# Kernel tuning notes

Hardware: AMD Instinct MI355X
Metric: run time of the kernel (lower is better)

## Reference

```python
import jax, jax.numpy as jnp
import numpy as np

B, D, H, O, RH, P = 8192, 784, 2048, 1024, 128, 64
NI = NJ = NK = 4  # input regions / hidden groups / output groups


def _make_groups():
    idx = np.arange(28 * 28).reshape(28, 28)
    input_groups = np.stack([
        idx[:14, :14].ravel(), idx[:14, 14:].ravel(),
        idx[14:, :14].ravel(), idx[14:, 14:].ravel(),
    ]).astype(np.int32)                                   # [4, 196]
    hidden_groups = np.arange(H, dtype=np.int32).reshape(NJ, H // NJ)   # [4, 512]
    output_groups = np.arange(O, dtype=np.int32).reshape(NK, O // NK)   # [4, 256]
    return input_groups, hidden_groups, output_groups


def setup_inputs() -> dict:
    key = jax.random.key(0)
    ks = jax.random.split(key, 9)
    ig, hg, og = _make_groups()
    inp = {
        "x":   jax.random.normal(ks[0], (B, D), jnp.float32),
        "W1":  jax.random.normal(ks[1], (H, D), jnp.float32) / np.sqrt(D),
        "b1":  jax.random.normal(ks[2], (H,), jnp.float32) * 0.01,
        "W2":  jax.random.normal(ks[3], (O, H), jnp.float32) / np.sqrt(H),
        "b2":  jax.random.normal(ks[4], (O,), jnp.float32) * 0.01,
        "Wr1": jax.random.normal(ks[5], (RH, D), jnp.float32) / np.sqrt(D),
        "br1": jax.random.normal(ks[6], (RH,), jnp.float32) * 0.01,
        "Wr2": jax.random.normal(ks[7], (P, RH), jnp.float32) / np.sqrt(RH),
        "br2": jax.random.normal(ks[8], (P,), jnp.float32) * 0.01,
        "input_groups": jnp.asarray(ig),
        "hidden_groups": jnp.asarray(hg),
        "output_groups": jnp.asarray(og),
        "top_k": 8,
    }
    return inp


def reference(x, W1, b1, W2, b2, Wr1, br1, Wr2, br2,
              input_groups, hidden_groups, output_groups, top_k):
    # --- router MLP (eval mode: dropout = identity, no routing noise) ---
    h_r = jax.nn.relu(x @ Wr1.T + br1)
    scores = h_r @ Wr2.T + br2                      # [B, P]
    probs = jax.nn.softmax(scores, axis=-1)         # temperature = 1.0

    # --- top-k pathway selection + renormalization ---
    top_vals, top_idx = jax.lax.top_k(probs, top_k)
    bsz = x.shape[0]
    mask = jnp.zeros_like(probs).at[jnp.arange(bsz)[:, None], top_idx].set(top_vals)
    wts = mask / (mask.sum(axis=-1, keepdims=True) + 1e-8)
    wts4 = wts.reshape(bsz, NI, NJ, NK)             # pathway_idx = i*16 + j*4 + k

    # --- gather pathway sub-blocks ---
    x_reg = x[:, input_groups]                      # [B, I, 196]
    # W1g[i, j] = W1[hidden_groups[j]][:, input_groups[i]] -> [I, J, 512, 196]
    W1g = W1[hidden_groups[None, :, :, None], input_groups[:, None, None, :]]
    b1g = b1[hidden_groups]                         # [J, 512]
    # W2g[j, k] = W2[output_groups[k]][:, hidden_groups[j]] -> [J, K, 256, 512]
    W2g = W2[output_groups[None, :, :, None], hidden_groups[:, None, None, :]]
    b2g = b2[output_groups]                         # [K, 256]

    # --- pathway computation (exact erf GELU, as torch F.gelu default) ---
    hidden = jax.nn.gelu(
        jnp.einsum('bin,ijhn->ijbh', x_reg, W1g) + b1g[None, :, None, :],
        approximate=False)                          # [I, J, B, 512]
    # weighted pathway outputs, contracted over i, j, h without materializing
    # the full [I, J, K, B, 256] tensor
    out_main = jnp.einsum('ijbh,jkoh,bijk->bko', hidden, W2g, wts4)  # [B, K, 256]
    wsum = wts4.sum(axis=(1, 2))                    # [B, K] (bias weighted per pathway)
    out_blocks = out_main + wsum[:, :, None] * b2g[None]

    out = jnp.zeros((bsz, O), x.dtype).at[:, output_groups].add(out_blocks)
    return out
```

## Files before the change

### kernel.cpp

```cpp
#include <hip/hip_runtime.h>
#include <hip/hip_bf16.h>
#include <hip/hip_fp16.h>

#define B_  8192
#define D_  784
#define H_  2048
#define O_  1024
#define RH_ 128
#define P_  64
#define KP  224
#define KC  196

typedef __attribute__((ext_vector_type(8))) short short8;
typedef __attribute__((ext_vector_type(4))) float f32x4;

__device__ inline float bf2f(unsigned short u) {
  union { unsigned int i; float f; } v; v.i = ((unsigned int)u) << 16; return v.f;
}
__device__ inline unsigned short f2bf(float f) {
  __hip_bfloat16 h = __float2bfloat16(f);
  return *reinterpret_cast<unsigned short*>(&h);
}
__device__ inline unsigned short f2h(float f) {
  __half h = __float2half(f);
  return *reinterpret_cast<unsigned short*>(&h);
}
__device__ inline float h2f(unsigned short u) {
  __half h = *reinterpret_cast<__half*>(&u);
  return __half2float(h);
}
__device__ inline float erf_fast(float x) {
  float ax = fabsf(x);
  float t = 1.0f / (1.0f + 0.3275911f * ax);
  float p = ((((1.061405429f * t - 1.453152027f) * t + 1.421413741f) * t
              - 0.284496736f) * t + 0.254829592f) * t;
  float y = 1.0f - p * __expf(-ax * ax);
  return x < 0.f ? -y : y;
}
__device__ inline float gelu_exact(float v) {
  return 0.5f * v * (1.0f + erf_fast(v * 0.70710678118654752f));
}

__device__ inline void gload_lds16(const void* g, void* l) {
  __builtin_amdgcn_global_load_lds((const __attribute__((address_space(1))) void*)g,
                                   (__attribute__((address_space(3))) void*)l, 16, 0, 0);
}

__device__ inline void gemm128_db(const unsigned short* gA0, const unsigned short* gA1,
                                  const unsigned short* gB0, const unsigned short* gB1,
                                  int K, char* lds, f32x4 acc[4][4]) {
  const int t = threadIdx.x;
  const int w = t >> 6, l = t & 63;
  const int wr = (w >> 1) * 64, wc = (w & 1) * 64;
  const int lr = l & 15;
  const int swr = (lr >> 1) & 3;
  const int arow = (wr + lr) * 64 + (((l >> 4) ^ swr) * 16);
  const int brow = 8192 + (wc + lr) * 64 + (((l >> 4) ^ swr) * 16);
  const int tOff = t * 16;
  {
    char* d = lds + tOff;
    gload_lds16(gA0, d);
    gload_lds16(gA1, d + 4096);
    gload_lds16(gB0, d + 8192);
    gload_lds16(gB1, d + 12288);
  }
  __syncthreads();
  int cur = 0;
  for (int kt = 0; kt < K; kt += 32) {
    const int nxt = kt + 32;
    if (nxt < K) {
      char* d = lds + ((cur ^ 1) << 14) + tOff;
      gload_lds16(gA0 + nxt, d);
      gload_lds16(gA1 + nxt, d + 4096);
      gload_lds16(gB0 + nxt, d + 8192);
      gload_lds16(gB1 + nxt, d + 12288);
    }
    __builtin_amdgcn_sched_barrier(0);
    const char* buf = lds + (cur << 14);
    short8 af[4], bfr[4];
#pragma unroll
    for (int f = 0; f < 4; ++f) {
      af[f]  = *(const short8*)(buf + arow + f * 1024);
      bfr[f] = *(const short8*)(buf + brow + f * 1024);
    }
#pragma unroll
    for (int fm = 0; fm < 4; ++fm)
#pragma unroll
      for (int fn = 0; fn < 4; ++fn)
        acc[fm][fn] = __builtin_amdgcn_mfma_f32_16x16x32_bf16(af[fm], bfr[fn], acc[fm][fn], 0, 0, 0);
    __syncthreads();
    cur ^= 1;
  }
}

__device__ inline void gemm128_db64(const unsigned short* gA0, const unsigned short* gA1,
                                    const unsigned short* gB0, const unsigned short* gB1,
                                    int K, char* lds, f32x4 acc[4][4]) {
  const int t = threadIdx.x;
  const int w = t >> 6, l = t & 63;
  const int wr = (w >> 1) * 64, wc = (w & 1) * 64;
  const int lr = l & 15;
  const int swr = (lr >> 1) & 3;
  const int arow = (wr + lr) * 64 + (((l >> 4) ^ swr) * 16);
  const int brow = 8192 + (wc + lr) * 64 + (((l >> 4) ^ swr) * 16);
  const int tOff = t * 16;
#define STAGE64(bufbase, ksrc) { \
    char* d = lds + (bufbase) + tOff; \
    gload_lds16(gA0 + (ksrc), d); \
    gload_lds16(gA1 + (ksrc), d + 4096); \
    gload_lds16(gB0 + (ksrc), d + 8192); \
    gload_lds16(gB1 + (ksrc), d + 12288); \
    gload_lds16(gA0 + (ksrc) + 32, d + 16384); \
    gload_lds16(gA1 + (ksrc) + 32, d + 16384 + 4096); \
    gload_lds16(gB0 + (ksrc) + 32, d + 16384 + 8192); \
    gload_lds16(gB1 + (ksrc) + 32, d + 16384 + 12288); \
  }
  STAGE64(0, 0);
  __syncthreads();
  int cur = 0;
  for (int kt = 0; kt < K; kt += 64) {
    if (kt + 64 < K) STAGE64((cur ^ 1) << 15, kt + 64);
    __builtin_amdgcn_sched_barrier(0);
    const char* buf = lds + (cur << 15);
#pragma unroll
    for (int c = 0; c < 2; ++c) {
      const char* ch = buf + c * 16384;
      short8 af[4], bfr[4];
#pragma unroll
      for (int f = 0; f < 4; ++f) {
        af[f]  = *(const short8*)(ch + arow + f * 1024);
        bfr[f] = *(const short8*)(ch + brow + f * 1024);
      }
#pragma unroll
      for (int fm = 0; fm < 4; ++fm)
#pragma unroll
        for (int fn = 0; fn < 4; ++fn)
          acc[fm][fn] = __builtin_amdgcn_mfma_f32_16x16x32_bf16(af[fm], bfr[fn], acc[fm][fn], 0, 0, 0);
    }
    __syncthreads();
    cur ^= 1;
  }
#undef STAGE64
}

__device__ inline void gemm128_bt64(const unsigned short* __restrict__ A,
                                    const unsigned short* __restrict__ Bm,
                                    int K, char* lds, f32x4 acc[4][4]) {
  const int t = threadIdx.x;
  const int s_orig = (t & 3) ^ ((t >> 3) & 3);
  const size_t srcOff = (size_t)(t >> 2) * K + s_orig * 8;
  gemm128_db64(A + srcOff, A + srcOff + (size_t)64 * K,
               Bm + srcOff, Bm + srcOff + (size_t)64 * K, K, lds, acc);
}

__global__ void k_prep(const float* __restrict__ x, const float* __restrict__ W1,
                       const float* __restrict__ W2, const int* __restrict__ ig,
                       unsigned short* __restrict__ xreg, unsigned short* __restrict__ w1g,
                       unsigned short* __restrict__ w2b) {
  const size_t N1 = (size_t)4 * B_ * KP;
  const size_t N2 = (size_t)4 * H_ * KP;
  const size_t N3 = (size_t)O_ * H_;
  const size_t TOT = N1 + N2 + N3;
  for (size_t idx = (size_t)blockIdx.x * blockDim.x + threadIdx.x; idx < TOT;
       idx += (size_t)gridDim.x * blockDim.x) {
    if (idx < N1) {
      int n = (int)(idx % KP); size_t r = idx / KP;
      int b = (int)(r % B_); int i = (int)(r / B_);
      float v = (n < 196) ? x[(size_t)b * D_ + ig[i * 196 + n]] : 0.f;
      xreg[idx] = f2bf(v);
    } else if (idx < N1 + N2) {
      size_t q = idx - N1;
      int n = (int)(q % KP); size_t r = q / KP;
      int h = (int)(r % H_); int i = (int)(r / H_);
      float v = (n < 196) ? W1[(size_t)h * D_ + ig[i * 196 + n]] : 0.f;
      w1g[q] = f2bf(v);
    } else {
      size_t q = idx - N1 - N2;
      w2b[q] = f2bf(W2[q]);
    }
  }
}

__global__ __launch_bounds__(256) void k_r1s(const float* __restrict__ x,
    const float* __restrict__ Wr1, const float* __restrict__ br1,
    float* __restrict__ hrp) {
  __shared__ float As[64][33];
  __shared__ float Bs[64][33];
  const int b0 = blockIdx.x * 64;
  const int h0 = blockIdx.y * 64;
  const int kb = blockIdx.z * KC;
  const int kend = kb + KC;
  const int t = threadIdx.x;
  const int srow = t >> 2;
  const int scol = (t & 3) * 8;
  const int ty = t >> 4, tx = t & 15;
  float acc[4][4];
#pragma unroll
  for (int i = 0; i < 4; ++i)
#pragma unroll
    for (int j = 0; j < 4; ++j) acc[i][j] = 0.f;
  const float* gA = x   + (size_t)(b0 + srow) * D_;
  const float* gB = Wr1 + (size_t)(h0 + srow) * D_;
  float4 a0 = *(const float4*)(gA + kb + scol);
  float4 a1 = *(const float4*)(gA + kb + scol + 4);
  float4 w0 = *(const float4*)(gB + kb + scol);
  float4 w1 = *(const float4*)(gB + kb + scol + 4);
  for (int k0 = kb; k0 < kend; k0 += 32) {
    __syncthreads();
    *(float4*)&As[srow][scol]     = a0;
    *(float4*)&As[srow][scol + 4] = a1;
    *(float4*)&Bs[srow][scol]     = w0;
    *(float4*)&Bs[srow][scol + 4] = w1;
    __syncthreads();
    const int kn = k0 + 32;
    if (kn < kend) {
      a0 = (kn + scol + 4 <= kend) ? *(const float4*)(gA + kn + scol)     : float4{0,0,0,0};
      a1 = (kn + scol + 8 <= kend) ? *(const float4*)(gA + kn + scol + 4) : float4{0,0,0,0};
      w0 = (kn + scol + 4 <= kend) ? *(const float4*)(gB + kn + scol)     : float4{0,0,0,0};
      w1 = (kn + scol + 8 <= kend) ? *(const float4*)(gB + kn + scol + 4) : float4{0,0,0,0};
    }
    __builtin_amdgcn_sched_barrier(0);
#pragma unroll
    for (int kk = 0; kk < 8; ++kk) {
      float4 a4[4], b4[4];
#pragma unroll
      for (int i = 0; i < 4; ++i) a4[i] = *(const float4*)&As[ty * 4 + i][kk * 4];
#pragma unroll
      for (int j = 0; j < 4; ++j) b4[j] = *(const float4*)&Bs[tx * 4 + j][kk * 4];
#pragma unroll
      for (int i = 0; i < 4; ++i)
#pragma unroll
        for (int j = 0; j < 4; ++j)
          acc[i][j] += a4[i].x * b4[j].x + a4[i].y * b4[j].y +
                       a4[i].z * b4[j].z + a4[i].w * b4[j].w;
    }
  }
  float* hz = hrp + (size_t)blockIdx.z * B_ * RH_;
#pragma unroll
  for (int j = 0; j < 4; ++j) {
    const int h = h0 + tx * 4 + j;
    const float bias = (blockIdx.z == 0) ? br1[h] : 0.f;
#pragma unroll
    for (int i = 0; i < 4; ++i)
      hz[(size_t)(b0 + ty * 4 + i) * RH_ + h] = acc[i][j] + bias;
  }
}

#define R2S 32
__global__ __launch_bounds__(256) void k_r2(const float* __restrict__ hrp,
    const float* __restrict__ Wr2, const float* __restrict__ br2,
    float* __restrict__ wts, float* __restrict__ wsum,
    unsigned long long* __restrict__ actmask) {
  __shared__ float Ws[64][130];
  __shared__ float hs[R2S][128];
  const int s0 = blockIdx.x * R2S;
  const int t = threadIdx.x;
  for (int idx = t; idx < 2048; idx += 256) {
    int r = idx >> 5, c = (idx & 31) * 4;
    *(float4*)&Ws[r][c] = *(const float4*)(Wr2 + (size_t)r * RH_ + c);
  }
  for (int idx = t; idx < R2S * 32; idx += 256) {
    int r = idx >> 5, c = (idx & 31) * 4;
    const size_t off = (size_t)(s0 + r) * RH_ + c;
    float4 p0 = *(const float4*)(hrp + off);
    float4 p1 = *(const float4*)(hrp + (size_t)1 * B_ * RH_ + off);
    float4 p2 = *(const float4*)(hrp + (size_t)2 * B_ * RH_ + off);
    float4 p3 = *(const float4*)(hrp + (size_t)3 * B_ * RH_ + off);
    float4 s;
    s.x = fmaxf(p0.x + p1.x + p2.x + p3.x, 0.f);
    s.y = fmaxf(p0.y + p1.y + p2.y + p3.y, 0.f);
    s.z = fmaxf(p0.z + p1.z + p2.z + p3.z, 0.f);
    s.w = fmaxf(p0.w + p1.w + p2.w + p3.w, 0.f);
    *(float4*)&hs[r][c] = s;
  }
  __syncthreads();
  const int w = t >> 6, p = t & 63;
  const float wb2 = br2[p];
  for (int si = 0; si < R2S / 4; ++si) {
    const int sl = w * (R2S / 4) + si;
    float sc = wb2;
#pragma unroll
    for (int kk = 0; kk < 32; ++kk) {
      float4 h4 = *(const float4*)&hs[sl][kk * 4];
      float4 w4 = *(const float4*)&Ws[p][kk * 4];
      sc += h4.x * w4.x + h4.y * w4.y + h4.z * w4.z + h4.w * w4.w;
    }
    float m = sc;
#pragma unroll
    for (int o = 32; o; o >>= 1) m = fmaxf(m, __shfl_xor(m, o));
    float e = __expf(sc - m);
    float Z = e;
#pragma unroll
    for (int o = 32; o; o >>= 1) Z += __shfl_xor(Z, o);
    bool sel = false;
    float ssum = 0.f;
    for (int it = 0; it < 8; ++it) {
      float v = sel ? -1.f : e;
      float vm = v;
#pragma unroll
      for (int o = 32; o; o >>= 1) vm = fmaxf(vm, __shfl_xor(vm, o));
      unsigned long long mask = __ballot(!sel && v == vm);
      int first = __ffsll((long long)mask) - 1;
      if (p == first) sel = true;
      ssum += vm;
    }
    const float dn = 1.0f / (ssum + 1e-8f * Z);
    const float wv = sel ? e * dn : 0.f;
    wts[(size_t)(s0 + sl) * 64 + p] = wv;
    const unsigned long long am = __ballot(sel);
    if (p == 0) actmask[s0 + sl] = am;
    float part = wv;
#pragma unroll
    for (int o = 4; o < 64; o <<= 1) part += __shfl_xor(part, o);
    if (p < 4) wsum[(size_t)(s0 + sl) * 4 + p] = part;
  }
}

__global__ __launch_bounds__(256) void k_compact(const unsigned long long* __restrict__ actmask,
                                                 int* __restrict__ lists,
                                                 int* __restrict__ counts) {
  __shared__ int wcnt[4];
  __shared__ int sbase;
  const int ij = blockIdx.x;
  const int shift = (ij >> 2) * 16 + (ij & 3) * 4;
  const int t = threadIdx.x;
  const int wid = t >> 6, lane = t & 63;
  unsigned long long mk[32];
#pragma unroll
  for (int c = 0; c < 32; ++c) mk[c] = actmask[c * 256 + t];
  if (t == 0) sbase = 0;
  __syncthreads();
  for (int c = 0; c < 32; ++c) {
    const int b = c * 256 + t;
    const bool act = ((mk[c] >> shift) & 0xFULL) != 0ULL;
    const unsigned long long m = __ballot(act);
    if (lane == 0) wcnt[wid] = __popcll(m);
    __syncthreads();
    int off = sbase;
    const int tot = wcnt[0] + wcnt[1] + wcnt[2] + wcnt[3];
    for (int q = 0; q < wid; ++q) off += wcnt[q];
    if (act)
      lists[ij * B_ + off + __popcll(m & ((1ULL << lane) - 1ULL))] = b;
    __syncthreads();
    if (t == 0) sbase += tot;
  }
  __syncthreads();
  if (t == 0) counts[ij] = sbase;
}

__global__ __launch_bounds__(256) void k_l1g(const unsigned short* __restrict__ xreg,
    const unsigned short* __restrict__ w1g, const float* __restrict__ b1,
    const int* __restrict__ lists, const int* __restrict__ counts,
    unsigned short* __restrict__ hid16) {
  const int mt = blockIdx.x, nt = blockIdx.y, iq = blockIdx.z;
  const int ij = iq * 4 + (nt >> 2);
  const int count = counts[ij];
  if (mt * 128 >= count) return;
  __shared__ __align__(128) char lds[32768];
  __shared__ int rows[128];
  const int t = threadIdx.x;
  const int* list = lists + (size_t)ij * B_;
  if (t < 128) {
    int rl = mt * 128 + t;
    rows[t] = list[rl < count ? rl : count - 1];
  }
  __syncthreads();
  const int s_orig = (t & 3) ^ ((t >> 3) & 3);
  const int scol = s_orig * 8;
  const int r0 = rows[t >> 2], r1 = rows[(t >> 2) + 64];
  const unsigned short* gA0 = xreg + ((size_t)iq * B_ + r0) * KP + scol;
  const unsigned short* gA1 = xreg + ((size_t)iq * B_ + r1) * KP + scol;
  const unsigned short* gB0 = w1g + ((size_t)(iq * H_ + nt * 128) + (t >> 2)) * KP + scol;
  const unsigned short* gB1 = gB0 + (size_t)64 * KP;
  f32x4 acc[4][4];
#pragma unroll
  for (int a = 0; a < 4; ++a)
#pragma unroll
    for (int b = 0; b < 4; ++b) acc[a][b] = (f32x4){0.f, 0.f, 0.f, 0.f};
  gemm128_db(gA0, gA1, gB0, gB1, KP, lds, acc);
  const int w = t >> 6, l = t & 63;
  const int rloc0 = (w >> 1) * 64 + (l >> 4) * 4;
  const int cloc = (w & 1) * 64 + (l & 15);
  unsigned short* lt = (unsigned short*)lds;
#pragma unroll
  for (int fn = 0; fn < 4; ++fn) {
    const int col = cloc + fn * 16;
    const float bias = b1[nt * 128 + col];
#pragma unroll
    for (int fm = 0; fm < 4; ++fm)
#pragma unroll
      for (int r = 0; r < 4; ++r) {
        const int row = rloc0 + fm * 16 + r;
        const int gsw = (col >> 3) ^ (row & 7);
        lt[row * 128 + gsw * 8 + (col & 7)] = f2h(acc[fm][fn][r] + bias);
      }
  }
  __syncthreads();
  const int mlim = count - mt * 128;
  const int row = t >> 1, half = t & 1;
  if (row < mlim) {
    unsigned short* dst = hid16 + ((size_t)iq * B_ + rows[row]) * H_ + nt * 128 + half * 64;
#pragma unroll
    for (int q = 0; q < 8; ++q) {
      const int g = (half * 8 + q) ^ (row & 7);
      *(short8*)(dst + q * 8) = *(const short8*)(lt + row * 128 + g * 8);
    }
  }
}

__global__ __launch_bounds__(256) void k_combine(unsigned short* __restrict__ hid,
                                                 const float* __restrict__ wts) {
  const int b = blockIdx.x;
  const int n = threadIdx.x * 8;
  const int j = n >> 9;
  const float* wb = wts + (size_t)b * 64 + j * 4;
  float acc[4][8];
#pragma unroll
  for (int k = 0; k < 4; ++k)
#pragma unroll
    for (int e = 0; e < 8; ++e) acc[k][e] = 0.f;
#pragma unroll
  for (int i = 0; i < 4; ++i) {
    const float4 w4 = *(const float4*)(wb + i * 16);
    if (w4.x != 0.f || w4.y != 0.f || w4.z != 0.f || w4.w != 0.f) {
      short8 raw = *(const short8*)(hid + ((size_t)i * B_ + b) * H_ + n);
#pragma unroll
      for (int e = 0; e < 8; ++e) {
        float g = gelu_exact(h2f((unsigned short)raw[e]));
        acc[0][e] += g * w4.x;
        acc[1][e] += g * w4.y;
        acc[2][e] += g * w4.z;
        acc[3][e] += g * w4.w;
      }
    }
  }
#pragma unroll
  for (int k = 0; k < 4; ++k) {
    short8 outv;
#pragma unroll
    for (int e = 0; e < 8; ++e) outv[e] = (short)f2bf(acc[k][e]);
    *(short8*)(hid + ((size_t)k * B_ + b) * H_ + n) = outv;
  }
}

__global__ __launch_bounds__(256) void k_l2(const unsigned short* __restrict__ G,
    const unsigned short* __restrict__ w2b, const float* __restrict__ b2,
    const float* __restrict__ wsum, float* __restrict__ out) {
  __shared__ __align__(128) char lds[65536];
  const int mt = blockIdx.x, nt = blockIdx.y, k = blockIdx.z;
  const unsigned short* A  = G + ((size_t)k * B_ + mt * 128) * H_;
  const unsigned short* Bm = w2b + ((size_t)(k * 256 + nt * 128)) * H_;
  f32x4 acc[4][4];
#pragma unroll
  for (int a = 0; a < 4; ++a)
#pragma unroll
    for (int b = 0; b < 4; ++b) acc[a][b] = (f32x4){0.f, 0.f, 0.f, 0.f};
  gemm128_bt64(A, Bm, H_, lds, acc);
  const int t = threadIdx.x, w = t >> 6, l = t & 63;
  const int rbase = mt * 128 + (w >> 1) * 64 + (l >> 4) * 4;
  const int cb = nt * 128 + (w & 1) * 64 + (l & 15);
#pragma unroll
  for (int fn = 0; fn < 4; ++fn) {
    const int ncol = k * 256 + cb + fn * 16;
    const float bias = b2[ncol];
#pragma unroll
    for (int fm = 0; fm < 4; ++fm)
#pragma unroll
      for (int r = 0; r < 4; ++r) {
        const int m = rbase + fm * 16 + r;
        out[(size_t)m * O_ + ncol] = acc[fm][fn][r] + wsum[m * 4 + k] * bias;
      }
  }
}

extern "C" void kernel_launch(void* const* d_in, const int* in_sizes, int n_in,
                              void* d_out, int out_size, void* d_ws, size_t ws_size,
                              hipStream_t stream) {
  const float* x   = (const float*)d_in[0];
  const float* W1  = (const float*)d_in[1];
  const float* b1  = (const float*)d_in[2];
  const float* W2  = (const float*)d_in[3];
  const float* b2  = (const float*)d_in[4];
  const float* Wr1 = (const float*)d_in[5];
  const float* br1 = (const float*)d_in[6];
  const float* Wr2 = (const float*)d_in[7];
  const float* br2 = (const float*)d_in[8];
  const int*   ig  = (const int*)d_in[9];
  float* out = (float*)d_out;
  char* ws = (char*)d_ws;
  unsigned short* xreg = (unsigned short*)(ws);
  unsigned short* w1g  = (unsigned short*)(ws + 14680064);
  unsigned short* w2b  = (unsigned short*)(ws + 18350080);
  float*          wts  = (float*)(ws + 22544384);
  float*          wsum = (float*)(ws + 24641536);
  unsigned short* hid  = (unsigned short*)(ws + 24772608);
  float*          hrp  = (float*)(ws + 24772608);
  int*                lists   = (int*)d_out;
  int*                counts  = lists + 16 * B_;
  unsigned long long* actmask = (unsigned long long*)((char*)d_out + 524352);

  k_prep<<<dim3(2048), dim3(256), 0, stream>>>(x, W1, W2, ig, xreg, w1g, w2b);
  k_r1s<<<dim3(B_ / 64, RH_ / 64, 4), dim3(256), 0, stream>>>(x, Wr1, br1, hrp);
  k_r2<<<dim3(B_ / R2S), dim3(256), 0, stream>>>(hrp, Wr2, br2, wts, wsum, actmask);
  k_compact<<<dim3(16), dim3(256), 0, stream>>>(actmask, lists, counts);
  k_l1g<<<dim3(B_ / 128, H_ / 128, 4), dim3(256), 0, stream>>>(xreg, w1g, b1, lists, counts, hid);
  k_combine<<<dim3(B_), dim3(256), 0, stream>>>(hid, wts);
  k_l2<<<dim3(B_ / 128, 2, 4), dim3(256), 0, stream>>>(hid, w2b, b2, wsum, out);
}
```

Before: 234.8 us.

## Compute router first layer with split-fp16 MFMA instead of fp32 FMA

Replaces the scalar fp32 router GEMM with an MFMA-based one. x and Wr1 are each split into hi and lo fp16 parts, and three products (xhi*Whi, xlo*Whi, xhi*Wlo) are computed as separate z-slices, which keeps near-fp32 accuracy. The router bias is now added in k_r2 instead of the GEMM, and the prep kernel writes the padded split operands. This costs extra prep work and workspace memory, in exchange for matrix-core throughput on the router matmul.

Measured after the change: 209.4 us. -10.8%, faster.

```diff
diff --git a/kernel.cpp b/kernel.cpp
--- a/kernel.cpp
+++ b/kernel.cpp
@@ -9,9 +9,10 @@
 #define RH_ 128
 #define P_  64
 #define KP  224
-#define KC  196
+#define KR  800
 
 typedef __attribute__((ext_vector_type(8))) short short8;
+typedef __attribute__((ext_vector_type(8))) _Float16 h16x8;
 typedef __attribute__((ext_vector_type(4))) float f32x4;
 
 __device__ inline float bf2f(unsigned short u) {
@@ -46,6 +47,7 @@
                                    (__attribute__((address_space(3))) void*)l, 16, 0, 0);
 }
 
+template <bool F16>
 __device__ inline void gemm128_db(const unsigned short* gA0, const unsigned short* gA1,
                                   const unsigned short* gB0, const unsigned short* gB1,
                                   int K, char* lds, f32x4 acc[4][4]) {
@@ -86,8 +88,13 @@
 #pragma unroll
     for (int fm = 0; fm < 4; ++fm)
 #pragma unroll
-      for (int fn = 0; fn < 4; ++fn)
-        acc[fm][fn] = __builtin_amdgcn_mfma_f32_16x16x32_bf16(af[fm], bfr[fn], acc[fm][fn], 0, 0, 0);
+      for (int fn = 0; fn < 4; ++fn) {
+        if constexpr (F16)
+          acc[fm][fn] = __builtin_amdgcn_mfma_f32_16x16x32_f16(
+              (h16x8)af[fm], (h16x8)bfr[fn], acc[fm][fn], 0, 0, 0);
+        else
+          acc[fm][fn] = __builtin_amdgcn_mfma_f32_16x16x32_bf16(af[fm], bfr[fn], acc[fm][fn], 0, 0, 0);
+      }
     __syncthreads();
     cur ^= 1;
   }
@@ -155,12 +162,16 @@
 
 __global__ void k_prep(const float* __restrict__ x, const float* __restrict__ W1,
                        const float* __restrict__ W2, const int* __restrict__ ig,
+                       const float* __restrict__ Wr1,
                        unsigned short* __restrict__ xreg, unsigned short* __restrict__ w1g,
-                       unsigned short* __restrict__ w2b) {
+                       unsigned short* __restrict__ w2b,
+                       unsigned short* __restrict__ xsp, unsigned short* __restrict__ wr1sp) {
   const size_t N1 = (size_t)4 * B_ * KP;
   const size_t N2 = (size_t)4 * H_ * KP;
   const size_t N3 = (size_t)O_ * H_;
-  const size_t TOT = N1 + N2 + N3;
+  const size_t N4 = (size_t)B_ * KR;
+  const size_t N5 = (size_t)RH_ * KR;
+  const size_t TOT = N1 + N2 + N3 + N4 + N5;
   for (size_t idx = (size_t)blockIdx.x * blockDim.x + threadIdx.x; idx < TOT;
        idx += (size_t)gridDim.x * blockDim.x) {
     if (idx < N1) {
@@ -174,80 +185,66 @@
       int h = (int)(r % H_); int i = (int)(r / H_);
       float v = (n < 196) ? W1[(size_t)h * D_ + ig[i * 196 + n]] : 0.f;
       w1g[q] = f2bf(v);
-    } else {
+    } else if (idx < N1 + N2 + N3) {
       size_t q = idx - N1 - N2;
       w2b[q] = f2bf(W2[q]);
-    }
-  }
-}
-
-__global__ __launch_bounds__(256) void k_r1s(const float* __restrict__ x,
-    const float* __restrict__ Wr1, const float* __restrict__ br1,
-    float* __restrict__ hrp) {
-  __shared__ float As[64][33];
-  __shared__ float Bs[64][33];
-  const int b0 = blockIdx.x * 64;
-  const int h0 = blockIdx.y * 64;
-  const int kb = blockIdx.z * KC;
-  const int kend = kb + KC;
-  const int t = threadIdx.x;
-  const int srow = t >> 2;
-  const int scol = (t & 3) * 8;
-  const int ty = t >> 4, tx = t & 15;
-  float acc[4][4];
-#pragma unroll
-  for (int i = 0; i < 4; ++i)
-#pragma unroll
-    for (int j = 0; j < 4; ++j) acc[i][j] = 0.f;
-  const float* gA = x   + (size_t)(b0 + srow) * D_;
-  const float* gB = Wr1 + (size_t)(h0 + srow) * D_;
-  float4 a0 = *(const float4*)(gA + kb + scol);
-  float4 a1 = *(const float4*)(gA + kb + scol + 4);
-  float4 w0 = *(const float4*)(gB + kb + scol);
-  float4 w1 = *(const float4*)(gB + kb + scol + 4);
-  for (int k0 = kb; k0 < kend; k0 += 32) {
-    __syncthreads();
-    *(float4*)&As[srow][scol]     = a0;
-    *(float4*)&As[srow][scol + 4] = a1;
-    *(float4*)&Bs[srow][scol]     = w0;
-    *(float4*)&Bs[srow][scol + 4] = w1;
-    __syncthreads();
-    const int kn = k0 + 32;
-    if (kn < kend) {
-      a0 = (kn + scol + 4 <= kend) ? *(const float4*)(gA + kn + scol)     : float4{0,0,0,0};
-      a1 = (kn + scol + 8 <= kend) ? *(const float4*)(gA + kn + scol + 4) : float4{0,0,0,0};
-      w0 = (kn + scol + 4 <= kend) ? *(const float4*)(gB + kn + scol)     : float4{0,0,0,0};
-      w1 = (kn + scol + 8 <= kend) ? *(const float4*)(gB + kn + scol + 4) : float4{0,0,0,0};
-    }
-    __builtin_amdgcn_sched_barrier(0);
-#pragma unroll
-    for (int kk = 0; kk < 8; ++kk) {
-      float4 a4[4], b4[4];
-#pragma unroll
-      for (int i = 0; i < 4; ++i) a4[i] = *(const float4*)&As[ty * 4 + i][kk * 4];
-#pragma unroll
-      for (int j = 0; j < 4; ++j) b4[j] = *(const float4*)&Bs[tx * 4 + j][kk * 4];
-#pragma unroll
-      for (int i = 0; i < 4; ++i)
-#pragma unroll
-        for (int j = 0; j < 4; ++j)
-          acc[i][j] += a4[i].x * b4[j].x + a4[i].y * b4[j].y +
-                       a4[i].z * b4[j].z + a4[i].w * b4[j].w;
-    }
-  }
-  float* hz = hrp + (size_t)blockIdx.z * B_ * RH_;
-#pragma unroll
-  for (int j = 0; j < 4; ++j) {
-    const int h = h0 + tx * 4 + j;
-    const float bias = (blockIdx.z == 0) ? br1[h] : 0.f;
-#pragma unroll
-    for (int i = 0; i < 4; ++i)
-      hz[(size_t)(b0 + ty * 4 + i) * RH_ + h] = acc[i][j] + bias;
+    } else if (idx < N1 + N2 + N3 + N4) {
+      size_t q = idx - N1 - N2 - N3;
+      int c = (int)(q % KR); int b = (int)(q / KR);
+      float v = (c < D_) ? x[(size_t)b * D_ + c] : 0.f;
+      unsigned short hi = f2h(v);
+      unsigned short lo = f2h(v - h2f(hi));
+      xsp[(size_t)b * (2 * KR) + c]      = hi;
+      xsp[(size_t)b * (2 * KR) + KR + c] = lo;
+    } else {
+      size_t q = idx - N1 - N2 - N3 - N4;
+      int c = (int)(q % KR); int h = (int)(q / KR);
+      float v = (c < D_) ? Wr1[(size_t)h * D_ + c] : 0.f;
+      unsigned short hi = f2h(v);
+      unsigned short lo = f2h(v - h2f(hi));
+      wr1sp[(size_t)h * KR + c]                    = hi;
+      wr1sp[(size_t)RH_ * KR + h * KR + c]         = hi;
+      wr1sp[(size_t)2 * RH_ * KR + h * KR + c]     = lo;
+    }
+  }
+}
+
+__global__ __launch_bounds__(256) void k_r1m(const unsigned short* __restrict__ xsp,
+    const unsigned short* __restrict__ wr1sp, float* __restrict__ hrp) {
+  __shared__ __align__(128) char lds[32768];
+  const int mt = blockIdx.x, z = blockIdx.y;
+  const int t = threadIdx.x;
+  const int aoff = (z == 1) ? KR : 0;
+  const int s_orig = (t & 3) ^ ((t >> 3) & 3);
+  const int scol = s_orig * 8;
+  const unsigned short* gA0 = xsp + ((size_t)(mt * 128) + (t >> 2)) * (2 * KR) + aoff + scol;
+  const unsigned short* gA1 = gA0 + (size_t)64 * (2 * KR);
+  const unsigned short* gB0 = wr1sp + (size_t)z * RH_ * KR + (size_t)(t >> 2) * KR + scol;
+  const unsigned short* gB1 = gB0 + (size_t)64 * KR;
+  f32x4 acc[4][4];
+#pragma unroll
+  for (int a = 0; a < 4; ++a)
+#pragma unroll
+    for (int b = 0; b < 4; ++b) acc[a][b] = (f32x4){0.f, 0.f, 0.f, 0.f};
+  gemm128_db<true>(gA0, gA1, gB0, gB1, KR, lds, acc);
+  float* hz = hrp + (size_t)z * B_ * RH_;
+  const int w = t >> 6, l = t & 63;
+  const int rbase = mt * 128 + (w >> 1) * 64 + (l >> 4) * 4;
+  const int cb = (w & 1) * 64 + (l & 15);
+#pragma unroll
+  for (int fn = 0; fn < 4; ++fn) {
+    const int h = cb + fn * 16;
+#pragma unroll
+    for (int fm = 0; fm < 4; ++fm)
+#pragma unroll
+      for (int r = 0; r < 4; ++r)
+        hz[(size_t)(rbase + fm * 16 + r) * RH_ + h] = acc[fm][fn][r];
   }
 }
 
 #define R2S 32
 __global__ __launch_bounds__(256) void k_r2(const float* __restrict__ hrp,
+    const float* __restrict__ br1,
     const float* __restrict__ Wr2, const float* __restrict__ br2,
     float* __restrict__ wts, float* __restrict__ wsum,
     unsigned long long* __restrict__ actmask) {
@@ -265,12 +262,12 @@
     float4 p0 = *(const float4*)(hrp + off);
     float4 p1 = *(const float4*)(hrp + (size_t)1 * B_ * RH_ + off);
     float4 p2 = *(const float4*)(hrp + (size_t)2 * B_ * RH_ + off);
-    float4 p3 = *(const float4*)(hrp + (size_t)3 * B_ * RH_ + off);
+    float4 bb = *(const float4*)(br1 + c);
     float4 s;
-    s.x = fmaxf(p0.x + p1.x + p2.x + p3.x, 0.f);
-    s.y = fmaxf(p0.y + p1.y + p2.y + p3.y, 0.f);
-    s.z = fmaxf(p0.z + p1.z + p2.z + p3.z, 0.f);
-    s.w = fmaxf(p0.w + p1.w + p2.w + p3.w, 0.f);
+    s.x = fmaxf(p0.x + p1.x + p2.x + bb.x, 0.f);
+    s.y = fmaxf(p0.y + p1.y + p2.y + bb.y, 0.f);
+    s.z = fmaxf(p0.z + p1.z + p2.z + bb.z, 0.f);
+    s.w = fmaxf(p0.w + p1.w + p2.w + bb.w, 0.f);
     *(float4*)&hs[r][c] = s;
   }
   __syncthreads();
@@ -377,7 +374,7 @@
   for (int a = 0; a < 4; ++a)
 #pragma unroll
     for (int b = 0; b < 4; ++b) acc[a][b] = (f32x4){0.f, 0.f, 0.f, 0.f};
-  gemm128_db(gA0, gA1, gB0, gB1, KP, lds, acc);
+  gemm128_db<false>(gA0, gA1, gB0, gB1, KP, lds, acc);
   const int w = t >> 6, l = t & 63;
   const int rloc0 = (w >> 1) * 64 + (l >> 4) * 4;
   const int cloc = (w & 1) * 64 + (l & 15);
@@ -494,14 +491,16 @@
   float*          wts  = (float*)(ws + 22544384);
   float*          wsum = (float*)(ws + 24641536);
   unsigned short* hid  = (unsigned short*)(ws + 24772608);
-  float*          hrp  = (float*)(ws + 24772608);
+  float*          hrp   = (float*)(ws + 24772608);
+  unsigned short* xsp   = (unsigned short*)(ws + 24772608 + 12582912);
+  unsigned short* wr1sp = (unsigned short*)(ws + 24772608 + 38797312);
   int*                lists   = (int*)d_out;
   int*                counts  = lists + 16 * B_;
   unsigned long long* actmask = (unsigned long long*)((char*)d_out + 524352);
 
-  k_prep<<<dim3(2048), dim3(256), 0, stream>>>(x, W1, W2, ig, xreg, w1g, w2b);
-  k_r1s<<<dim3(B_ / 64, RH_ / 64, 4), dim3(256), 0, stream>>>(x, Wr1, br1, hrp);
-  k_r2<<<dim3(B_ / R2S), dim3(256), 0, stream>>>(hrp, Wr2, br2, wts, wsum, actmask);
+  k_prep<<<dim3(2048), dim3(256), 0, stream>>>(x, W1, W2, ig, Wr1, xreg, w1g, w2b, xsp, wr1sp);
+  k_r1m<<<dim3(B_ / 128, 3), dim3(256), 0, stream>>>(xsp, wr1sp, hrp);
+  k_r2<<<dim3(B_ / R2S), dim3(256), 0, stream>>>(hrp, br1, Wr2, br2, wts, wsum, actmask);
   k_compact<<<dim3(16), dim3(256), 0, stream>>>(actmask, lists, counts);
   k_l1g<<<dim3(B_ / 128, H_ / 128, 4), dim3(256), 0, stream>>>(xreg, w1g, b1, lists, counts, hid);
   k_combine<<<dim3(B_), dim3(256), 0, stream>>>(hid, wts);
```
